# Kernel tuning notes

Hardware: AMD Instinct MI355X
Metric: run time of the kernel (lower is better)

Reference implementation:

```python
import jax, jax.numpy as jnp
import numpy as np

N = 100000
FEAT = 256
HID = 128
OUT = 64
E = 1600000


def setup_inputs() -> dict:
    key = jax.random.key(0)
    ks = jax.random.split(key, 8)
    x = jax.random.normal(ks[0], (N, FEAT), dtype=jnp.float32)
    edge_index = jax.random.randint(ks[1], (2, E), 0, N, dtype=jnp.int64)
    # Glorot-like weights, zero bias (PyG GCNConv default init style)
    def glorot(k, fin, fout):
        s = (6.0 / (fin + fout)) ** 0.5
        return jax.random.uniform(k, (fin, fout), jnp.float32, -s, s)
    return {
        "x": x,
        "edge_index": edge_index,
        "W1": glorot(ks[2], FEAT, HID), "b1": jnp.zeros((HID,), jnp.float32),
        "W2": glorot(ks[3], HID, HID), "b2": jnp.zeros((HID,), jnp.float32),
        "W3": glorot(ks[4], HID, OUT), "b3": jnp.zeros((OUT,), jnp.float32),
    }


def _gcn_prep(edge_index, n_nodes):
    # Add self-loops and compute symmetric normalization deg^-1/2 (PyG gcn_norm).
    loops = jnp.arange(n_nodes, dtype=edge_index.dtype)
    src = jnp.concatenate([edge_index[0], loops])
    dst = jnp.concatenate([edge_index[1], loops])
    ones = jnp.ones(src.shape[0], dtype=jnp.float32)
    deg = jax.ops.segment_sum(ones, dst, num_segments=n_nodes)
    dinv = jnp.where(deg > 0, jax.lax.rsqrt(jnp.maximum(deg, 1.0)), 0.0)
    norm = dinv[src] * dinv[dst]  # [E+N]
    return src, dst, norm


def _gcn_layer(x, src, dst, norm, W, b, n_nodes):
    h = x @ W                              # [N, F_out]
    msg = h[src] * norm[:, None]           # gather + edge scale
    out = jax.ops.segment_sum(msg, dst, num_segments=n_nodes)  # scatter-add
    return out + b


def reference(x, edge_index, W1, b1, W2, b2, W3, b3):
    n = x.shape[0]
    src, dst, norm = _gcn_prep(edge_index, n)
    h = jax.nn.relu(_gcn_layer(x, src, dst, norm, W1, b1, n))
    h = jax.nn.relu(_gcn_layer(h, src, dst, norm, W2, b2, n))
    return _gcn_layer(h, src, dst, norm, W3, b3, n)
```

## Files before the change

kernel.cpp:

```cpp
#include <hip/hip_runtime.h>
#include <hip/hip_bf16.h>


#define NNODES 100000
#define NB 391
#define PB 2048
#define BCAP 12288

typedef _Float16 half8  __attribute__((ext_vector_type(8)));
typedef _Float16 half4v __attribute__((ext_vector_type(4)));
typedef _Float16 half2v __attribute__((ext_vector_type(2)));
typedef float    floatx4 __attribute__((ext_vector_type(4)));

static __device__ __forceinline__ floatx4 h2f4(half4v v) {
    return (floatx4){(float)v.x, (float)v.y, (float)v.z, (float)v.w};
}

__global__ __launch_bounds__(256) void blockhist_k(const int* __restrict__ dst,
                                                   int* __restrict__ H, int e) {
    __shared__ int h[NB];
    for (int q = threadIdx.x; q < NB; q += 256) h[q] = 0;
    __syncthreads();
    int base = blockIdx.x * PB;
    int lim = e - base; if (lim > PB) lim = PB;
    for (int i = threadIdx.x; i < lim; i += 256)
        atomicAdd(&h[dst[base + i] >> 8], 1);
    __syncthreads();
    for (int q = threadIdx.x; q < NB; q += 256)
        H[(size_t)blockIdx.x * NB + q] = h[q];
}

__global__ __launch_bounds__(256) void bucketscan_k(const int* __restrict__ H,
                                                    int* __restrict__ O,
                                                    int* __restrict__ T, int npb) {
    __shared__ int lds[256];
    int b = blockIdx.x, t = threadIdx.x;
    int running = 0;
    for (int c0 = 0; c0 < npb; c0 += 256) {
        int idx = c0 + t;
        int v = (idx < npb) ? H[(size_t)idx * NB + b] : 0;
        lds[t] = v;
        __syncthreads();
        #pragma unroll
        for (int off = 1; off < 256; off <<= 1) {
            int u = (t >= off) ? lds[t - off] : 0;
            __syncthreads();
            lds[t] += u;
            __syncthreads();
        }
        int excl = lds[t] - v + running;
        if (idx < npb) O[(size_t)idx * NB + b] = excl;
        running += lds[255];
        __syncthreads();
    }
    if (t == 0) T[b] = running;
}

__global__ __launch_bounds__(512) void scanT_k(const int* __restrict__ T,
                                               int* __restrict__ bbase, int e) {
    __shared__ int lds[512];
    int t = threadIdx.x;
    int v = (t < NB) ? T[t] : 0;
    lds[t] = v;
    __syncthreads();
    #pragma unroll
    for (int off = 1; off < 512; off <<= 1) {
        int u = (t >= off) ? lds[t - off] : 0;
        __syncthreads();
        lds[t] += u;
        __syncthreads();
    }
    if (t < NB) bbase[t] = lds[t] - v;
    if (t == 0) bbase[NB] = e;
}

__global__ __launch_bounds__(256) void scatter_k(const int* __restrict__ src,
                                                 const int* __restrict__ dst,
                                                 const int* __restrict__ O,
                                                 const int* __restrict__ bbase,
                                                 unsigned* __restrict__ binned, int e) {
    __shared__ int cur[NB];
    for (int q = threadIdx.x; q < NB; q += 256)
        cur[q] = bbase[q] + O[(size_t)blockIdx.x * NB + q];
    __syncthreads();
    int base = blockIdx.x * PB;
    int lim = e - base; if (lim > PB) lim = PB;
    for (int i = threadIdx.x; i < lim; i += 256) {
        int d = dst[base + i];
        int s = src[base + i];
        int p = atomicAdd(&cur[d >> 8], 1);
        binned[p] = ((unsigned)(d & 255) << 17) | (unsigned)s;
    }
}

__global__ __launch_bounds__(256) void bucket_fill_k(
    const unsigned* __restrict__ binned, const int* __restrict__ bbase,
    int* __restrict__ rowptr, int* __restrict__ eidx,
    float* __restrict__ dinv, int n, int e) {
    __shared__ int cnt[256];
    __shared__ int cur[256];
    __shared__ int lds[256];
    __shared__ int sbuf[BCAP];
    int b = blockIdx.x, t = threadIdx.x;
    int beg = bbase[b], end = bbase[b + 1];
    int m = end - beg;
    cnt[t] = 0;
    __syncthreads();
    for (int q = t; q < m; q += 256) {
        unsigned r = binned[beg + q];
        atomicAdd(&cnt[r >> 17], 1);
    }
    __syncthreads();
    int v = cnt[t];
    lds[t] = v;
    __syncthreads();
    #pragma unroll
    for (int off = 1; off < 256; off <<= 1) {
        int u = (t >= off) ? lds[t - off] : 0;
        __syncthreads();
        lds[t] += u;
        __syncthreads();
    }
    int excl = lds[t] - v;
    int node = b * 256 + t;
    if (node < n) {
        rowptr[node] = beg + excl;
        dinv[node] = rsqrtf(1.0f + (float)v);
    }
    if (b == NB - 1 && t == 0) rowptr[n] = e;
    cur[t] = excl;
    __syncthreads();
    for (int q = t; q < m; q += 256) {
        unsigned r = binned[beg + q];
        int p = atomicAdd(&cur[r >> 17], 1);
        if (p < BCAP) sbuf[p] = (int)(r & 0x1FFFFu);
    }
    __syncthreads();
    for (int q = t; q < m; q += 256) eidx[beg + q] = sbuf[q];
}

__global__ __launch_bounds__(256) void castWt_k(
    const float* __restrict__ W1, const float* __restrict__ W2,
    const float* __restrict__ W3, _Float16* __restrict__ Wt1,
    _Float16* __restrict__ Wt2, _Float16* __restrict__ Wt3) {
    int i = blockIdx.x * 256 + threadIdx.x;
    if (i < 128 * 256) {
        int nn = i >> 8, k = i & 255;
        Wt1[i] = (_Float16)W1[k * 128 + nn];
    }
    if (i < 128 * 128) {
        int nn = i >> 7, k = i & 127;
        Wt2[i] = (_Float16)W2[k * 128 + nn];
    }
    if (i < 64 * 128) {
        int nn = i >> 7, k = i & 127;
        Wt3[i] = (_Float16)W3[k * 64 + nn];
    }
}

template<typename TA, int FIN, int FOUT>
__global__ __launch_bounds__(256) void gemm_reg_k(
    const TA* __restrict__ X, const _Float16* __restrict__ Wt,
    const float* __restrict__ dinv, _Float16* __restrict__ G, int n)
{
    constexpr int NCT = FOUT / 64;
    constexpr int NKC = FIN / 32;
    const int tid  = threadIdx.x;
    const int wave = tid >> 6;
    const int lane = tid & 63;
    const int mrow = lane & 15;
    const int kq   = (lane >> 4) * 8;
    const int m0   = blockIdx.x * 64;

    half8 bfr[NCT][NKC];
    #pragma unroll
    for (int ct = 0; ct < NCT; ++ct) {
        const _Float16* wp = Wt + (size_t)((wave * NCT + ct) * 16 + mrow) * FIN + kq;
        #pragma unroll
        for (int kc = 0; kc < NKC; ++kc)
            bfr[ct][kc] = *(const half8*)(wp + kc * 32);
    }

    const TA* ap[4];
    #pragma unroll
    for (int rt = 0; rt < 4; ++rt) {
        int r = m0 + rt * 16 + mrow;
        if (r > n - 1) r = n - 1;
        ap[rt] = X + (size_t)r * FIN + kq;
    }

    auto lda = [&](const TA* p) -> half8 {
        if constexpr (sizeof(TA) == 2) {
            return *(const half8*)p;
        } else {
            float4 u0 = *(const float4*)p;
            float4 u1 = *(const float4*)(p + 4);
            return (half8){(_Float16)u0.x, (_Float16)u0.y, (_Float16)u0.z, (_Float16)u0.w,
                           (_Float16)u1.x, (_Float16)u1.y, (_Float16)u1.z, (_Float16)u1.w};
        }
    };

    floatx4 acc[4][NCT];
    #pragma unroll
    for (int rt = 0; rt < 4; ++rt)
        #pragma unroll
        for (int ct = 0; ct < NCT; ++ct) acc[rt][ct] = (floatx4){0.f, 0.f, 0.f, 0.f};

    half8 a_cur[4], a_nxt[4];
    #pragma unroll
    for (int rt = 0; rt < 4; ++rt) a_cur[rt] = lda(ap[rt]);

    #pragma unroll
    for (int kc = 0; kc < NKC; ++kc) {
        if (kc + 1 < NKC) {
            #pragma unroll
            for (int rt = 0; rt < 4; ++rt) a_nxt[rt] = lda(ap[rt] + (kc + 1) * 32);
        }
        #pragma unroll
        for (int rt = 0; rt < 4; ++rt)
            #pragma unroll
            for (int ct = 0; ct < NCT; ++ct)
                acc[rt][ct] = __builtin_amdgcn_mfma_f32_16x16x32_f16(
                    a_cur[rt], bfr[ct][kc], acc[rt][ct], 0, 0, 0);
        #pragma unroll
        for (int rt = 0; rt < 4; ++rt) a_cur[rt] = a_nxt[rt];
    }

    #pragma unroll
    for (int rt = 0; rt < 4; ++rt) {
        #pragma unroll
        for (int reg = 0; reg < 4; ++reg) {
            int r = m0 + rt * 16 + (lane >> 4) * 4 + reg;
            if (r < n) {
                float s = dinv[r];
                #pragma unroll
                for (int ct = 0; ct < NCT; ++ct) {
                    G[(size_t)r * FOUT + (wave * NCT + ct) * 16 + mrow] =
                        (_Float16)(acc[rt][ct][reg] * s);
                }
            }
        }
    }
}

template<bool RELU, typename OutT>
__global__ __launch_bounds__(256) void gather128_k(
    const _Float16* __restrict__ g, const int* __restrict__ rowptr,
    const int* __restrict__ eidx, const float* __restrict__ dinv,
    const float* __restrict__ bias, OutT* __restrict__ out, int n)
{
    int wave = threadIdx.x >> 6;
    int lane = threadIdx.x & 63;
    int half = lane >> 5;
    int hl   = lane & 31;
    int node = blockIdx.x * 4 + wave;
    if (node >= n) return;

    int beg = rowptr[node];
    int end = rowptr[node + 1];

    const half4v* g4 = (const half4v*)g;
    floatx4 aA = {0.f,0.f,0.f,0.f}, aB = aA, aC = aA, aD = aA;
    if (half == 0) aA = h2f4(g4[(size_t)node * 32 + hl]);

    for (int j0 = beg; j0 < end; j0 += 64) {
        int m = end - j0; if (m > 64) m = 64;
        int id = (lane < m) ? eidx[j0 + lane] : 0;
        int t = 0;
        for (; t + 7 < m; t += 8) {
            int i0 = __shfl(id, t + half);
            int i1 = __shfl(id, t + 2 + half);
            int i2 = __shfl(id, t + 4 + half);
            int i3 = __shfl(id, t + 6 + half);
            half4v v0 = g4[(size_t)i0 * 32 + hl];
            half4v v1 = g4[(size_t)i1 * 32 + hl];
            half4v v2 = g4[(size_t)i2 * 32 + hl];
            half4v v3 = g4[(size_t)i3 * 32 + hl];
            aA += h2f4(v0); aB += h2f4(v1); aC += h2f4(v2); aD += h2f4(v3);
        }
        for (; t + 1 < m; t += 2) {
            int i0 = __shfl(id, t + half);
            aA += h2f4(g4[(size_t)i0 * 32 + hl]);
        }
        if (t < m) {
            int i0 = __shfl(id, t);
            if (half == 0) aA += h2f4(g4[(size_t)i0 * 32 + hl]);
        }
    }
    aA += aB; aC += aD; aA += aC;
    aA.x += __shfl_down(aA.x, 32);
    aA.y += __shfl_down(aA.y, 32);
    aA.z += __shfl_down(aA.z, 32);
    aA.w += __shfl_down(aA.w, 32);

    if (half == 0) {
        float sc = dinv[node];
        float4 bb = *(const float4*)(bias + 4 * hl);
        float o0 = fmaf(aA.x, sc, bb.x);
        float o1 = fmaf(aA.y, sc, bb.y);
        float o2 = fmaf(aA.z, sc, bb.z);
        float o3 = fmaf(aA.w, sc, bb.w);
        if (RELU) {
            o0 = fmaxf(o0, 0.f); o1 = fmaxf(o1, 0.f);
            o2 = fmaxf(o2, 0.f); o3 = fmaxf(o3, 0.f);
        }
        if constexpr (sizeof(OutT) == 2) {
            ((half4v*)out)[(size_t)node * 32 + hl] =
                (half4v){(_Float16)o0, (_Float16)o1, (_Float16)o2, (_Float16)o3};
        } else {
            *(float4*)((float*)out + (size_t)node * 128 + 4 * hl) =
                make_float4(o0, o1, o2, o3);
        }
    }
}

template<bool RELU>
__global__ __launch_bounds__(256) void gather64_k(
    const _Float16* __restrict__ g, const int* __restrict__ rowptr,
    const int* __restrict__ eidx, const float* __restrict__ dinv,
    const float* __restrict__ bias, float* __restrict__ out, int n)
{
    int wave = threadIdx.x >> 6;
    int lane = threadIdx.x & 63;
    int half = lane >> 5;
    int hl   = lane & 31;
    int node = blockIdx.x * 4 + wave;
    if (node >= n) return;

    int beg = rowptr[node];
    int end = rowptr[node + 1];

    const half2v* g2 = (const half2v*)g;
    float ax=0.f, ay=0.f, bx=0.f, by=0.f, cx=0.f, cy=0.f, dx=0.f, dy=0.f;
    if (half == 0) {
        half2v v = g2[(size_t)node * 32 + hl];
        ax = (float)v.x; ay = (float)v.y;
    }

    for (int j0 = beg; j0 < end; j0 += 64) {
        int m = end - j0; if (m > 64) m = 64;
        int id = (lane < m) ? eidx[j0 + lane] : 0;
        int t = 0;
        for (; t + 7 < m; t += 8) {
            int i0 = __shfl(id, t + half);
            int i1 = __shfl(id, t + 2 + half);
            int i2 = __shfl(id, t + 4 + half);
            int i3 = __shfl(id, t + 6 + half);
            half2v v0 = g2[(size_t)i0 * 32 + hl];
            half2v v1 = g2[(size_t)i1 * 32 + hl];
            half2v v2 = g2[(size_t)i2 * 32 + hl];
            half2v v3 = g2[(size_t)i3 * 32 + hl];
            ax += (float)v0.x; ay += (float)v0.y;
            bx += (float)v1.x; by += (float)v1.y;
            cx += (float)v2.x; cy += (float)v2.y;
            dx += (float)v3.x; dy += (float)v3.y;
        }
        for (; t + 1 < m; t += 2) {
            int i0 = __shfl(id, t + half);
            half2v v0 = g2[(size_t)i0 * 32 + hl];
            ax += (float)v0.x; ay += (float)v0.y;
        }
        if (t < m) {
            int i0 = __shfl(id, t);
            if (half == 0) {
                half2v v0 = g2[(size_t)i0 * 32 + hl];
                ax += (float)v0.x; ay += (float)v0.y;
            }
        }
    }
    ax += bx + cx + dx; ay += by + cy + dy;
    ax += __shfl_down(ax, 32);
    ay += __shfl_down(ay, 32);

    if (half == 0) {
        float sc = dinv[node];
        float2 bb = *(const float2*)(bias + 2 * hl);
        float ox = fmaf(ax, sc, bb.x);
        float oy = fmaf(ay, sc, bb.y);
        if (RELU) { ox = fmaxf(ox, 0.f); oy = fmaxf(oy, 0.f); }
        *(float2*)(out + (size_t)node * 64 + 2 * hl) = make_float2(ox, oy);
    }
}

extern "C" void kernel_launch(void* const* d_in, const int* in_sizes, int n_in,
                              void* d_out, int out_size, void* d_ws, size_t ws_size,
                              hipStream_t stream) {
    const float* x  = (const float*)d_in[0];
    const int*   ei = (const int*)d_in[1];
    const float* W1 = (const float*)d_in[2];
    const float* b1 = (const float*)d_in[3];
    const float* W2 = (const float*)d_in[4];
    const float* b2 = (const float*)d_in[5];
    const float* W3 = (const float*)d_in[6];
    const float* b3 = (const float*)d_in[7];
    float* out = (float*)d_out;

    const int N = NNODES;
    const int E = in_sizes[1] / 2;
    const int* srcI = ei;
    const int* dstI = ei + E;

    const int npb = (E + PB - 1) / PB;

    char* ws = (char*)d_ws;
    size_t p = 0;
    auto alloc = [&](size_t bytes) { void* r = ws + p; p = (p + bytes + 255) & ~(size_t)255; return r; };
    float*     dinv   = (float*)    alloc((size_t)N * 4);
    int*       rowptr = (int*)      alloc((size_t)(N + 1) * 4);
    int*       bbase  = (int*)      alloc((size_t)(NB + 1) * 4);
    int*       T      = (int*)      alloc((size_t)NB * 4);
    int*       H      = (int*)      alloc((size_t)npb * NB * 4);
    int*       O      = (int*)      alloc((size_t)npb * NB * 4);
    unsigned*  binned = (unsigned*) alloc((size_t)E * 4);
    int*       eidx   = (int*)      alloc((size_t)E * 4);
    _Float16*  Wt1    = (_Float16*) alloc((size_t)128 * 256 * 2);
    _Float16*  Wt2    = (_Float16*) alloc((size_t)128 * 128 * 2);
    _Float16*  Wt3    = (_Float16*) alloc((size_t)64 * 128 * 2);
    _Float16*  A      = (_Float16*) alloc((size_t)N * 128 * 2);
    _Float16*  Ch     = (_Float16*) alloc((size_t)N * 128 * 2);

    const int nb_node4 = (N + 3) / 4;
    const int nb_gemm = (N + 63) / 64;

    blockhist_k<<<npb, 256, 0, stream>>>(dstI, H, E);
    castWt_k<<<128, 256, 0, stream>>>(W1, W2, W3, Wt1, Wt2, Wt3);
    bucketscan_k<<<NB, 256, 0, stream>>>(H, O, T, npb);
    scanT_k<<<1, 512, 0, stream>>>(T, bbase, E);
    scatter_k<<<npb, 256, 0, stream>>>(srcI, dstI, O, bbase, binned, E);
    bucket_fill_k<<<NB, 256, 0, stream>>>(binned, bbase, rowptr, eidx, dinv, N, E);

    gemm_reg_k<float, 256, 128><<<nb_gemm, 256, 0, stream>>>(x, Wt1, dinv, A, N);
    gather128_k<true, _Float16><<<nb_node4, 256, 0, stream>>>(A, rowptr, eidx, dinv, b1, Ch, N);

    gemm_reg_k<_Float16, 128, 128><<<nb_gemm, 256, 0, stream>>>(Ch, Wt2, dinv, A, N);
    gather128_k<true, _Float16><<<nb_node4, 256, 0, stream>>>(A, rowptr, eidx, dinv, b2, Ch, N);

    gemm_reg_k<_Float16, 128, 64><<<nb_gemm, 256, 0, stream>>>(Ch, Wt3, dinv, A, N);
    gather64_k<false><<<nb_node4, 256, 0, stream>>>(A, rowptr, eidx, dinv, b3, out, N);
}
```

Before: 488.5 us.

## Shrink GEMM tile to 16 rows per block and load all A fragments upfront

The dense transform kernel now handles 16 rows per block instead of 64. Each wave issues all of its A-fragment loads at once rather than software-pipelining four row tiles, and the launch bound asks for two blocks per CU. The aim is more blocks and memory parallelism with fewer registers per thread. The cost is that every block reloads the full weight fragment set, four times more often than before, and each MFMA chain is shorter.

New measurement: 525.3 us. 7.6% more time.

```diff
diff --git a/kernel.cpp b/kernel.cpp
--- a/kernel.cpp
+++ b/kernel.cpp
@@ -159,86 +159,69 @@
 }
 
 template<typename TA, int FIN, int FOUT>
-__global__ __launch_bounds__(256) void gemm_reg_k(
+__global__ __launch_bounds__(256, 2) void gemm_wave_k(
     const TA* __restrict__ X, const _Float16* __restrict__ Wt,
     const float* __restrict__ dinv, _Float16* __restrict__ G, int n)
 {
+    constexpr int NKC = FIN / 32;
     constexpr int NCT = FOUT / 64;
-    constexpr int NKC = FIN / 32;
-    const int tid  = threadIdx.x;
-    const int wave = tid >> 6;
-    const int lane = tid & 63;
+    const int wave = threadIdx.x >> 6;
+    const int lane = threadIdx.x & 63;
     const int mrow = lane & 15;
     const int kq   = (lane >> 4) * 8;
-    const int m0   = blockIdx.x * 64;
-
-    half8 bfr[NCT][NKC];
+    const int m0   = blockIdx.x * 16;
+
+    int r = m0 + mrow; if (r > n - 1) r = n - 1;
+
+    half8 af[NKC];
+    if constexpr (sizeof(TA) == 4) {
+        const float* xp = (const float*)X + (size_t)r * FIN + kq;
+        float4 t[2 * NKC];
+        #pragma unroll
+        for (int kc = 0; kc < NKC; ++kc) {
+            t[2 * kc]     = *(const float4*)(xp + kc * 32);
+            t[2 * kc + 1] = *(const float4*)(xp + kc * 32 + 4);
+        }
+        #pragma unroll
+        for (int kc = 0; kc < NKC; ++kc) {
+            float4 u0 = t[2 * kc], u1 = t[2 * kc + 1];
+            af[kc] = (half8){(_Float16)u0.x, (_Float16)u0.y, (_Float16)u0.z, (_Float16)u0.w,
+                             (_Float16)u1.x, (_Float16)u1.y, (_Float16)u1.z, (_Float16)u1.w};
+        }
+    } else {
+        const _Float16* xp = (const _Float16*)X + (size_t)r * FIN + kq;
+        #pragma unroll
+        for (int kc = 0; kc < NKC; ++kc)
+            af[kc] = *(const half8*)(xp + kc * 32);
+    }
+
+    half8 bf[NCT][NKC];
     #pragma unroll
     for (int ct = 0; ct < NCT; ++ct) {
         const _Float16* wp = Wt + (size_t)((wave * NCT + ct) * 16 + mrow) * FIN + kq;
         #pragma unroll
         for (int kc = 0; kc < NKC; ++kc)
-            bfr[ct][kc] = *(const half8*)(wp + kc * 32);
-    }
-
-    const TA* ap[4];
-    #pragma unroll
-    for (int rt = 0; rt < 4; ++rt) {
-        int r = m0 + rt * 16 + mrow;
-        if (r > n - 1) r = n - 1;
-        ap[rt] = X + (size_t)r * FIN + kq;
-    }
-
-    auto lda = [&](const TA* p) -> half8 {
-        if constexpr (sizeof(TA) == 2) {
-            return *(const half8*)p;
-        } else {
-            float4 u0 = *(const float4*)p;
-            float4 u1 = *(const float4*)(p + 4);
-            return (half8){(_Float16)u0.x, (_Float16)u0.y, (_Float16)u0.z, (_Float16)u0.w,
-                           (_Float16)u1.x, (_Float16)u1.y, (_Float16)u1.z, (_Float16)u1.w};
-        }
-    };
-
-    floatx4 acc[4][NCT];
-    #pragma unroll
-    for (int rt = 0; rt < 4; ++rt)
-        #pragma unroll
-        for (int ct = 0; ct < NCT; ++ct) acc[rt][ct] = (floatx4){0.f, 0.f, 0.f, 0.f};
-
-    half8 a_cur[4], a_nxt[4];
-    #pragma unroll
-    for (int rt = 0; rt < 4; ++rt) a_cur[rt] = lda(ap[rt]);
-
-    #pragma unroll
-    for (int kc = 0; kc < NKC; ++kc) {
-        if (kc + 1 < NKC) {
-            #pragma unroll
-            for (int rt = 0; rt < 4; ++rt) a_nxt[rt] = lda(ap[rt] + (kc + 1) * 32);
-        }
-        #pragma unroll
-        for (int rt = 0; rt < 4; ++rt)
+            bf[ct][kc] = *(const half8*)(wp + kc * 32);
+    }
+
+    floatx4 acc[NCT];
+    #pragma unroll
+    for (int ct = 0; ct < NCT; ++ct) acc[ct] = (floatx4){0.f, 0.f, 0.f, 0.f};
+    #pragma unroll
+    for (int kc = 0; kc < NKC; ++kc)
+        #pragma unroll
+        for (int ct = 0; ct < NCT; ++ct)
+            acc[ct] = __builtin_amdgcn_mfma_f32_16x16x32_f16(af[kc], bf[ct][kc], acc[ct], 0, 0, 0);
+
+    #pragma unroll
+    for (int reg = 0; reg < 4; ++reg) {
+        int rr = m0 + (lane >> 4) * 4 + reg;
+        if (rr < n) {
+            float s = dinv[rr];
             #pragma unroll
             for (int ct = 0; ct < NCT; ++ct)
-                acc[rt][ct] = __builtin_amdgcn_mfma_f32_16x16x32_f16(
-                    a_cur[rt], bfr[ct][kc], acc[rt][ct], 0, 0, 0);
-        #pragma unroll
-        for (int rt = 0; rt < 4; ++rt) a_cur[rt] = a_nxt[rt];
-    }
-
-    #pragma unroll
-    for (int rt = 0; rt < 4; ++rt) {
-        #pragma unroll
-        for (int reg = 0; reg < 4; ++reg) {
-            int r = m0 + rt * 16 + (lane >> 4) * 4 + reg;
-            if (r < n) {
-                float s = dinv[r];
-                #pragma unroll
-                for (int ct = 0; ct < NCT; ++ct) {
-                    G[(size_t)r * FOUT + (wave * NCT + ct) * 16 + mrow] =
-                        (_Float16)(acc[rt][ct][reg] * s);
-                }
-            }
+                G[(size_t)rr * FOUT + (wave * NCT + ct) * 16 + mrow] =
+                    (_Float16)(acc[ct][reg] * s);
         }
     }
 }
@@ -420,7 +403,7 @@
     _Float16*  Ch     = (_Float16*) alloc((size_t)N * 128 * 2);
 
     const int nb_node4 = (N + 3) / 4;
-    const int nb_gemm = (N + 63) / 64;
+    const int nb_gemm = (N + 15) / 16;
 
     blockhist_k<<<npb, 256, 0, stream>>>(dstI, H, E);
     castWt_k<<<128, 256, 0, stream>>>(W1, W2, W3, Wt1, Wt2, Wt3);
@@ -429,12 +412,12 @@
     scatter_k<<<npb, 256, 0, stream>>>(srcI, dstI, O, bbase, binned, E);
     bucket_fill_k<<<NB, 256, 0, stream>>>(binned, bbase, rowptr, eidx, dinv, N, E);
 
-    gemm_reg_k<float, 256, 128><<<nb_gemm, 256, 0, stream>>>(x, Wt1, dinv, A, N);
+    gemm_wave_k<float, 256, 128><<<nb_gemm, 256, 0, stream>>>(x, Wt1, dinv, A, N);
     gather128_k<true, _Float16><<<nb_node4, 256, 0, stream>>>(A, rowptr, eidx, dinv, b1, Ch, N);
 
-    gemm_reg_k<_Float16, 128, 128><<<nb_gemm, 256, 0, stream>>>(Ch, Wt2, dinv, A, N);
+    gemm_wave_k<_Float16, 128, 128><<<nb_gemm, 256, 0, stream>>>(Ch, Wt2, dinv, A, N);
     gather128_k<true, _Float16><<<nb_node4, 256, 0, stream>>>(A, rowptr, eidx, dinv, b2, Ch, N);
 
-    gemm_reg_k<_Float16, 128, 64><<<nb_gemm, 256, 0, stream>>>(Ch, Wt3, dinv, A, N);
+    gemm_wave_k<_Float16, 128, 64><<<nb_gemm, 256, 0, stream>>>(Ch, Wt3, dinv, A, N);
     gather64_k<false><<<nb_node4, 256, 0, stream>>>(A, rowptr, eidx, dinv, b3, out, N);
 }
```
